# Optimization experiments

Hardware: AMD Instinct MI355X
Metric: run time of the kernel (lower is better)

Reference implementation:

```python
import jax, jax.numpy as jnp
import numpy as np

PD = 3                      # spatial feature dim (z, y, x)
HB = 1024                   # hash base per lattice coordinate
HOFF = 512                  # offset: lattice coords assumed in [-512, 511]
FILL = np.int32(2**31 - 1)  # sentinel for padded hash slots
EPS = 2.220446049250313e-16 # np.finfo('float').eps as in the torch module

def _elev_mat():
    # Embedding onto hyperplane sum(x)=0 with std-dev scale factors
    # (canonical permutohedral-lattice elevation, Adams et al.).
    E = np.zeros((PD + 1, PD), np.float32)
    E[0] = 1.0
    for i in range(1, PD + 1):
        E[i, i - 1] = -i
        E[i, i:] = 1.0
    inv_std = np.sqrt(2.0 / 3.0) * (PD + 1)
    scale = inv_std / np.sqrt(np.arange(1, PD + 1) * np.arange(2, PD + 2))
    return (E * scale[None, :]).astype(np.float32)

_EMAT = _elev_mat()
_IU = np.triu(np.ones((PD + 1, PD + 1), bool), 1)   # j > i
_IL = np.tril(np.ones((PD + 1, PD + 1), bool), -1)  # j < i

def _hash(k):  # (..., PD) int32 -> (...,) int32, injective for |coord| < 512
    return ((k[..., 0] + HOFF) * HB + (k[..., 1] + HOFF)) * HB + (k[..., 2] + HOFF)

def permutohedral(values, features):
    """Splat-blur-slice Gaussian filter. values (N,VD), features (N,PD)."""
    N, VD = values.shape
    elevated = features @ jnp.asarray(_EMAT).T                  # (N, PD+1)
    # nearest remainder-0 lattice point (nearest multiple of PD+1, ties -> down)
    v = elevated / (PD + 1)
    up, down = jnp.ceil(v), jnp.floor(v)
    rem0 = jnp.where(up - v < v - down, up, down) * (PD + 1)
    diff = elevated - rem0
    lt = diff[:, :, None] < diff[:, None, :]
    le = diff[:, :, None] <= diff[:, None, :]
    rank = (lt & _IU).sum(-1) + (le & _IL).sum(-1)              # (N, PD+1) int32
    rank = rank + jnp.round(rem0.sum(-1) / (PD + 1)).astype(rank.dtype)[:, None]
    shift = jnp.where(rank < 0, PD + 1, 0) + jnp.where(rank > PD, -(PD + 1), 0)
    rank = rank + shift
    rem0 = rem0 + shift.astype(rem0.dtype)
    # barycentric coordinates inside the enclosing simplex
    t = (elevated - rem0) / (PD + 1)                            # (N, PD+1)
    ohA = jax.nn.one_hot(PD - rank, PD + 2, dtype=values.dtype)
    ohB = jax.nn.one_hot(PD + 1 - rank, PD + 2, dtype=values.dtype)
    b = (ohA * t[..., None]).sum(1) - (ohB * t[..., None]).sum(1)
    b = b.at[:, 0].add(1.0 + b[:, PD + 1])
    bary = b[:, :PD + 1]                                        # (N, PD+1)
    # keys of the PD+1 simplex vertices (first PD coords; last is implied)
    rem0i = rem0[:, :PD].astype(jnp.int32)
    ranki = rank[:, :PD].astype(jnp.int32)
    r = jnp.arange(PD + 1, dtype=jnp.int32)[None, :, None]
    keys = rem0i[:, None, :] + jnp.where(ranki[:, None, :] >= PD + 1 - r, r - (PD + 1), r)  # (N,PD+1,PD)
    h = _hash(keys).reshape(-1)                                 # (N*(PD+1),)
    M = h.shape[0]
    uh, inv = jnp.unique(h, size=M, fill_value=FILL, return_inverse=True)
    inv = inv.reshape(-1)
    # splat
    contrib = (values[:, None, :] * bary[:, :, None]).reshape(M, VD)
    lat = jax.ops.segment_sum(contrib, inv, num_segments=M)     # (M, VD)
    # decode unique keys from the (invertible) hash
    k2 = uh % HB - HOFF
    tq = uh // HB
    k1 = tq % HB - HOFF
    k0 = tq // HB - HOFF
    ukeys = jnp.stack([k0, k1, k2], -1).astype(jnp.int32)       # (M, PD)
    valid = (uh != FILL)[:, None]
    # blur with [0.5, 1, 0.5] along each of the PD+1 lattice directions
    def lookup(nk, lat_):
        nh = _hash(nk)
        idx = jnp.clip(jnp.searchsorted(uh, nh), 0, M - 1)
        ok = (uh[idx] == nh)[:, None]
        return jnp.where(ok, lat_[idx], 0.0)
    for j in range(PD + 1):
        o = np.ones(PD, np.int32)
        if j < PD:
            o[j] = -PD
        o = jnp.asarray(o)
        lat = jnp.where(valid, lat + 0.5 * (lookup(ukeys + o, lat) + lookup(ukeys - o, lat)), 0.0)
    # slice
    alpha = 1.0 / (1.0 + 2.0 ** (-PD))
    return alpha * jnp.einsum('nr,nrv->nv', bary, lat[inv.reshape(-1, PD + 1)])

def spatial_features(image, v_gamma, sigma_gamma):
    _, d, h, w = image.shape
    z = jnp.arange(d, dtype=jnp.float32)[:, None, None]
    y = jnp.arange(h, dtype=jnp.float32)[None, :, None]
    x = jnp.arange(w, dtype=jnp.float32)[None, None, :]
    zz = v_gamma[0] * jnp.broadcast_to(z, (d, h, w)) / sigma_gamma[0]
    xx = v_gamma[1] * jnp.broadcast_to(x, (d, h, w)) / sigma_gamma[1]
    yy = v_gamma[2] * jnp.broadcast_to(y, (d, h, w)) / sigma_gamma[2]
    return jnp.stack([zz, yy, xx], axis=3)                      # (d,h,w,3)

def setup_inputs() -> dict:
    key = jax.random.key(0)
    k1, k2 = jax.random.split(key)
    C, D, H, W = 4, 64, 128, 128
    return {
        'input_': jax.random.normal(k1, (C, D, H, W), jnp.float32),
        'image': jax.random.normal(k2, (1, D, H, W), jnp.float32),
        'v_gamma': jnp.ones((3,), jnp.float32),       # nn.Parameter init [1,1,1]
        'sigma_gamma': 5.0 * jnp.ones((3,), jnp.float32),
    }

def reference(input_, image, v_gamma, sigma_gamma):
    C, d, h, w = input_.shape
    N = d * h * w
    feats = spatial_features(image, v_gamma, sigma_gamma).reshape(N, PD)
    # filter q and the all-ones normalizer in one pass (linear per channel)
    vals = jnp.concatenate([input_.reshape(C, N).T, jnp.ones((N, 1), jnp.float32)], axis=1)
    out = permutohedral(vals, feats)
    q = out[:, :C].T.reshape(C, d, h, w)
    norm = out[:, C].reshape(1, d, h, w)
    return q * (1.0 / (norm + EPS))
```

## Files before the change

kernel.cpp:

```cpp
#include <hip/hip_runtime.h>


#define DD    64
#define HHH   128
#define WWW   128
#define NPTS  (DD * HHH * WWW)
#define LATN  (1 << 17)
#define LATF  (LATN * 5)
#define SH_BITS 10
#define SHSZ (1 << SH_BITS)
#define BLURBLK 64

__device__ __forceinline__ int encK(int K0, int K1, int K2) {
    return ((K2 >> 2) << 12) | ((K1 >> 2) << 7) | ((K0 >> 2) << 2) | (K0 & 3);
}

__device__ __forceinline__ void pl_geom(int z, int y, int x,
                                        const float* __restrict__ vg,
                                        const float* __restrict__ sg,
                                        int* didx, float* bout) {
    float f0 = vg[0] * (float)z / sg[0];
    float f1 = vg[2] * (float)y / sg[2];
    float f2 = vg[1] * (float)x / sg[1];

    const float m00 = (float)2.3094010767585034;
    const float m01 = (float)1.3333333333333333;
    const float m02 = (float)0.9428090415820634;
    const float m21 = (float)-2.6666666666666665;
    const float m32 = (float)-2.8284271247461903;

    float e[4];
    e[0] =  m00 * f0 + m01 * f1 + m02 * f2;
    e[1] = -m00 * f0 + m01 * f1 + m02 * f2;
    e[2] =  m21 * f1 + m02 * f2;
    e[3] =  m32 * f2;

    float rem0[4];
    int sumr = 0;
    #pragma unroll
    for (int i = 0; i < 4; ++i) {
        float v = e[i] * 0.25f;
        float up = ceilf(v), dn = floorf(v);
        float rr = ((up - v) < (v - dn)) ? up : dn;
        rem0[i] = rr * 4.0f;
        sumr += (int)rem0[i];
    }
    sumr /= 4;

    float diff[4];
    #pragma unroll
    for (int i = 0; i < 4; ++i) diff[i] = e[i] - rem0[i];
    int rank[4] = {0, 0, 0, 0};
    #pragma unroll
    for (int i = 0; i < 4; ++i)
        #pragma unroll
        for (int j = i + 1; j < 4; ++j) {
            if (diff[i] < diff[j]) rank[i]++; else rank[j]++;
        }

    #pragma unroll
    for (int i = 0; i < 4; ++i) {
        rank[i] += sumr;
        if (rank[i] < 0)      { rank[i] += 4; rem0[i] += 4.0f; }
        else if (rank[i] > 3) { rank[i] -= 4; rem0[i] -= 4.0f; }
    }

    float b[5] = {0.f, 0.f, 0.f, 0.f, 0.f};
    #pragma unroll
    for (int i = 0; i < 4; ++i) {
        float t = (e[i] - rem0[i]) * 0.25f;
        b[3 - rank[i]] += t;
        b[4 - rank[i]] -= t;
    }
    b[0] += 1.0f + b[4];

    int k0 = (int)rem0[0], k1 = (int)rem0[1], k2 = (int)rem0[2];
    #pragma unroll
    for (int r = 0; r < 4; ++r) {
        int o0 = (rank[0] >= 4 - r) ? (r - 4) : r;
        int o1 = (rank[1] >= 4 - r) ? (r - 4) : r;
        int o2 = (rank[2] >= 4 - r) ? (r - 4) : r;
        int K0 = (k0 + o0 + 16) & 127;
        int K1 = (k1 + o1 + 48) & 127;
        int K2 = (k2 + o2 + 88) & 127;
        didx[r] = encK(K0, K1, K2);
        bout[r] = b[r];
    }
}

__device__ __forceinline__ void pl_claim(int key, unsigned int* __restrict__ exists,
                                         int* __restrict__ wcnt, int* __restrict__ wl) {
    if (atomicExch(&exists[key], 1u) == 0u) {
        int p = atomicAdd(wcnt, 1);
        wl[p] = key;
    }
}

__device__ __forceinline__ void pl_emit(int key, const float* a,
                                        int* skey, float (*sacc)[5],
                                        float* __restrict__ latc,
                                        unsigned int* __restrict__ exists,
                                        int* __restrict__ wcnt, int* __restrict__ wl) {
    unsigned idx = ((unsigned)key * 2654435761u) >> (32 - SH_BITS);
    int probes = 0;
    bool inlds = true;
    for (;;) {
        int cur = skey[idx];
        if (cur == key) break;
        if (cur == -1) {
            cur = atomicCAS(&skey[idx], -1, key);
            if (cur == -1 || cur == key) break;
        }
        idx = (idx + 1) & (SHSZ - 1);
        if (++probes >= SHSZ) { inlds = false; break; }
    }
    if (inlds) {
        #pragma unroll
        for (int c = 0; c < 5; ++c) atomicAdd(&sacc[idx][c], a[c]);
    } else {
        float* L = latc + (size_t)key * 5;
        #pragma unroll
        for (int c = 0; c < 5; ++c) atomicAdd(L + c, a[c]);
        pl_claim(key, exists, wcnt, wl);
    }
}

__global__ __launch_bounds__(512, 4)
void pl_splat(const float* __restrict__ vals, const float* __restrict__ vg,
              const float* __restrict__ sg, float* __restrict__ latc,
              unsigned int* __restrict__ exists,
              int* __restrict__ wcnt, int* __restrict__ wl) {
    __shared__ int   skey[SHSZ];
    __shared__ float sacc[SHSZ][5];
    for (int i = threadIdx.x; i < SHSZ; i += 512) {
        skey[i] = -1;
        #pragma unroll
        for (int c = 0; c < 5; ++c) sacc[i][c] = 0.f;
    }
    __syncthreads();

    float* mycopy = latc + (size_t)(blockIdx.x & 3) * LATF;

    int bt = blockIdx.x;
    int xs = threadIdx.x & 7;
    int ly = (threadIdx.x >> 3) & 15;
    int lz = threadIdx.x >> 7;
    int xsl = ((xs & 3) << 1) | (xs >> 2);
    int x0 = ((bt & 3) << 5) + (xsl << 2);
    int y  = (((bt >> 2) & 7) << 4) + ly;
    int z  = ((bt >> 5) << 2) + lz;
    int n0 = (z << 14) + (y << 7) + x0;

    float4 q0 = *(const float4*)(vals + n0);
    float4 q1 = *(const float4*)(vals + NPTS + n0);
    float4 q2 = *(const float4*)(vals + 2 * NPTS + n0);
    float4 q3 = *(const float4*)(vals + 3 * NPTS + n0);
    float ch0[4] = {q0.x, q0.y, q0.z, q0.w};
    float ch1[4] = {q1.x, q1.y, q1.z, q1.w};
    float ch2[4] = {q2.x, q2.y, q2.z, q2.w};
    float ch3[4] = {q3.x, q3.y, q3.z, q3.w};

    int ckey[4];
    float acc[4][5];
    {
        int didx[4]; float b[4];
        pl_geom(z, y, x0, vg, sg, didx, b);
        #pragma unroll
        for (int r = 0; r < 4; ++r) {
            ckey[r] = didx[r];
            float w = b[r];
            acc[r][0] = w * ch0[0]; acc[r][1] = w * ch1[0];
            acc[r][2] = w * ch2[0]; acc[r][3] = w * ch3[0];
            acc[r][4] = w;
        }
    }
    #pragma unroll
    for (int p = 1; p < 4; ++p) {
        int didx[4]; float b[4];
        pl_geom(z, y, x0 + p, vg, sg, didx, b);
        #pragma unroll
        for (int r = 0; r < 4; ++r) {
            float w = b[r];
            if (didx[r] == ckey[r]) {
                acc[r][0] += w * ch0[p]; acc[r][1] += w * ch1[p];
                acc[r][2] += w * ch2[p]; acc[r][3] += w * ch3[p];
                acc[r][4] += w;
            } else {
                pl_emit(ckey[r], acc[r], skey, sacc, mycopy, exists, wcnt, wl);
                ckey[r] = didx[r];
                acc[r][0] = w * ch0[p]; acc[r][1] = w * ch1[p];
                acc[r][2] = w * ch2[p]; acc[r][3] = w * ch3[p];
                acc[r][4] = w;
            }
        }
    }
    #pragma unroll
    for (int r = 0; r < 4; ++r)
        pl_emit(ckey[r], acc[r], skey, sacc, mycopy, exists, wcnt, wl);

    __syncthreads();

    int rot = (blockIdx.x * 131) & (SHSZ - 1);
    for (int ii = threadIdx.x; ii < SHSZ; ii += 512) {
        int i = (ii + rot) & (SHSZ - 1);
        int key = skey[i];
        if (key < 0) continue;
        pl_claim(key, exists, wcnt, wl);
        float* L = mycopy + (size_t)key * 5;
        #pragma unroll
        for (int c = 0; c < 5; ++c) atomicAdd(L + c, sacc[i][c]);
    }
}

__global__ __launch_bounds__(256)
void pl_blur(const unsigned int* __restrict__ exists,
             const int* __restrict__ wl, const int* __restrict__ wcnt,
             const float* __restrict__ in, float* __restrict__ out,
             int d0, int d1, int d2, int first) {
    int cnt = *wcnt;
    for (int i = blockIdx.x * 256 + threadIdx.x; i < cnt; i += BLURBLK * 256) {
        int didx = wl[i];
        int r  = didx & 3;
        int K0 = (((didx >> 2)  & 31) << 2) | r;
        int K1 = (((didx >> 7)  & 31) << 2) | r;
        int K2 = (((didx >> 12) & 31) << 2) | r;
        float a[5];
        size_t o = (size_t)didx * 5;
        if (first) {
            #pragma unroll
            for (int c = 0; c < 5; ++c)
                a[c] = in[o + c] + in[LATF + o + c] +
                       in[2 * LATF + o + c] + in[3 * LATF + o + c];
        } else {
            #pragma unroll
            for (int c = 0; c < 5; ++c) a[c] = in[o + c];
        }
        #pragma unroll
        for (int sgn = 0; sgn < 2; ++sgn) {
            int P0 = K0 + (sgn ? -d0 : d0);
            int P1 = K1 + (sgn ? -d1 : d1);
            int P2 = K2 + (sgn ? -d2 : d2);
            if (((unsigned)P0 < 128u) & ((unsigned)P1 < 128u) & ((unsigned)P2 < 128u)) {
                int nk = encK(P0, P1, P2);
                if (exists[nk]) {
                    size_t no = (size_t)nk * 5;
                    if (first) {
                        #pragma unroll
                        for (int c = 0; c < 5; ++c)
                            a[c] += 0.5f * (in[no + c] + in[LATF + no + c] +
                                            in[2 * LATF + no + c] + in[3 * LATF + no + c]);
                    } else {
                        #pragma unroll
                        for (int c = 0; c < 5; ++c) a[c] += 0.5f * in[no + c];
                    }
                }
            }
        }
        #pragma unroll
        for (int c = 0; c < 5; ++c) out[o + c] = a[c];
    }
}

__global__ __launch_bounds__(256)
void pl_slice(const float* __restrict__ vg, const float* __restrict__ sg,
              const float* __restrict__ lat, float* __restrict__ out) {
    int n = blockIdx.x * 256 + threadIdx.x;
    if (n >= NPTS) return;
    int z = n >> 14;
    int y = (n >> 7) & 127;
    int x = n & 127;
    int didx[4]; float b[4];
    pl_geom(z, y, x, vg, sg, didx, b);
    float a0 = 0.f, a1 = 0.f, a2 = 0.f, a3 = 0.f, a4 = 0.f;
    #pragma unroll
    for (int r = 0; r < 4; ++r) {
        float w = b[r];
        const float* L = lat + (size_t)didx[r] * 5;
        a0 += w * L[0]; a1 += w * L[1]; a2 += w * L[2]; a3 += w * L[3]; a4 += w * L[4];
    }
    const float alpha = (float)(1.0 / 1.125);
    float norm = alpha * a4 + (float)2.220446049250313e-16;
    float invn = 1.0f / norm;
    out[n]            = (alpha * a0) * invn;
    out[NPTS + n]     = (alpha * a1) * invn;
    out[2 * NPTS + n] = (alpha * a2) * invn;
    out[3 * NPTS + n] = (alpha * a3) * invn;
}

extern "C" void kernel_launch(void* const* d_in, const int* in_sizes, int n_in,
                              void* d_out, int out_size, void* d_ws, size_t ws_size,
                              hipStream_t stream) {
    const float* input = (const float*)d_in[0];
    const float* vg = (const float*)d_in[2];
    const float* sg = (const float*)d_in[3];
    float* out = (float*)d_out;

    char* ws = (char*)d_ws;
    float* latc = (float*)ws;
    unsigned int* exists = (unsigned int*)(latc + (size_t)4 * LATF);
    int* wcnt = (int*)(exists + LATN);
    int*   wl = (int*)(wcnt + 64);
    float* A  = (float*)(wl + LATN);
    float* B  = A + LATF;

    size_t zbytes = (size_t)4 * LATF * 4 + (size_t)LATN * 4 + 256;
    hipMemsetAsync(ws, 0, zbytes, stream);

    pl_splat<<<512, dim3(512), 0, stream>>>(input, vg, sg, latc, exists, wcnt, wl);

    pl_blur<<<BLURBLK, dim3(256), 0, stream>>>(exists, wl, wcnt, latc, A, -3, 1, 1, 1);
    pl_blur<<<BLURBLK, dim3(256), 0, stream>>>(exists, wl, wcnt, A, B, 1, -3, 1, 0);
    pl_blur<<<BLURBLK, dim3(256), 0, stream>>>(exists, wl, wcnt, B, A, 1, 1, -3, 0);
    pl_blur<<<BLURBLK, dim3(256), 0, stream>>>(exists, wl, wcnt, A, B, 1, 1, 1, 0);

    pl_slice<<<NPTS / 256, dim3(256), 0, stream>>>(vg, sg, B, out);
}
```

Before: 191.2 us.

## Replace LDS hash splat with dense tile grid and fuse three blur passes

The splat kernel drops the per-block LDS open-addressing hash in favour of a dense 7x7x7x4 local lattice window. Each tile computes its window base analytically, accumulates with LDS atomics plus a bitmask, and falls back to global atomics for points outside the window. The last three blur passes are fused into one kernel that recomputes neighbour values recursively (p1f/p2f), which removes two launches and the intermediate round trips but causes heavy redundant gathers (about 27 reads per output channel). The blur is also parallelised per channel element, and the grid sizes change.

```diff
diff --git a/kernel.cpp b/kernel.cpp
--- a/kernel.cpp
+++ b/kernel.cpp
@@ -7,9 +7,9 @@
 #define NPTS  (DD * HHH * WWW)
 #define LATN  (1 << 17)
 #define LATF  (LATN * 5)
-#define SH_BITS 10
-#define SHSZ (1 << SH_BITS)
-#define BLURBLK 64
+#define DQ    7
+#define CELLS (DQ * DQ * DQ * 4)
+#define MASKW ((CELLS + 31) / 32)
 
 __device__ __forceinline__ int encK(int K0, int K1, int K2) {
     return ((K2 >> 2) << 12) | ((K1 >> 2) << 7) | ((K0 >> 2) << 2) | (K0 & 3);
@@ -18,7 +18,7 @@
 __device__ __forceinline__ void pl_geom(int z, int y, int x,
                                         const float* __restrict__ vg,
                                         const float* __restrict__ sg,
-                                        int* didx, float* bout) {
+                                        int* Kout , float* bout) {
     float f0 = vg[0] * (float)z / sg[0];
     float f1 = vg[2] * (float)y / sg[2];
     float f2 = vg[1] * (float)x / sg[1];
@@ -74,16 +74,15 @@
     }
     b[0] += 1.0f + b[4];
 
-    int k0 = (int)rem0[0], k1 = (int)rem0[1], k2 = (int)rem0[2];
+    int k0 = (int)rem0[0] + 16, k1 = (int)rem0[1] + 48, k2 = (int)rem0[2] + 88;
     #pragma unroll
     for (int r = 0; r < 4; ++r) {
         int o0 = (rank[0] >= 4 - r) ? (r - 4) : r;
         int o1 = (rank[1] >= 4 - r) ? (r - 4) : r;
         int o2 = (rank[2] >= 4 - r) ? (r - 4) : r;
-        int K0 = (k0 + o0 + 16) & 127;
-        int K1 = (k1 + o1 + 48) & 127;
-        int K2 = (k2 + o2 + 88) & 127;
-        didx[r] = encK(K0, K1, K2);
+        Kout[r * 3 + 0] = k0 + o0;
+        Kout[r * 3 + 1] = k1 + o1;
+        Kout[r * 3 + 2] = k2 + o2;
         bout[r] = b[r];
     }
 }
@@ -96,59 +95,47 @@
     }
 }
 
-__device__ __forceinline__ void pl_emit(int key, const float* a,
-                                        int* skey, float (*sacc)[5],
-                                        float* __restrict__ latc,
-                                        unsigned int* __restrict__ exists,
-                                        int* __restrict__ wcnt, int* __restrict__ wl) {
-    unsigned idx = ((unsigned)key * 2654435761u) >> (32 - SH_BITS);
-    int probes = 0;
-    bool inlds = true;
-    for (;;) {
-        int cur = skey[idx];
-        if (cur == key) break;
-        if (cur == -1) {
-            cur = atomicCAS(&skey[idx], -1, key);
-            if (cur == -1 || cur == key) break;
-        }
-        idx = (idx + 1) & (SHSZ - 1);
-        if (++probes >= SHSZ) { inlds = false; break; }
-    }
-    if (inlds) {
-        #pragma unroll
-        for (int c = 0; c < 5; ++c) atomicAdd(&sacc[idx][c], a[c]);
-    } else {
-        float* L = latc + (size_t)key * 5;
-        #pragma unroll
-        for (int c = 0; c < 5; ++c) atomicAdd(L + c, a[c]);
-        pl_claim(key, exists, wcnt, wl);
-    }
-}
-
-__global__ __launch_bounds__(512, 4)
+__device__ __forceinline__ void gl_add5(float* __restrict__ L, const float* a) {
+    #pragma unroll
+    for (int c = 0; c < 5; ++c) atomicAdd(L + c, a[c]);
+}
+
+__global__ __launch_bounds__(256, 4)
 void pl_splat(const float* __restrict__ vals, const float* __restrict__ vg,
               const float* __restrict__ sg, float* __restrict__ latc,
               unsigned int* __restrict__ exists,
               int* __restrict__ wcnt, int* __restrict__ wl) {
-    __shared__ int   skey[SHSZ];
-    __shared__ float sacc[SHSZ][5];
-    for (int i = threadIdx.x; i < SHSZ; i += 512) {
-        skey[i] = -1;
-        #pragma unroll
-        for (int c = 0; c < 5; ++c) sacc[i][c] = 0.f;
-    }
+    __shared__ float sacc[CELLS * 5];
+    __shared__ unsigned int smask[MASKW];
+    for (int i = threadIdx.x; i < CELLS * 5; i += 256) sacc[i] = 0.f;
+    for (int i = threadIdx.x; i < MASKW; i += 256) smask[i] = 0u;
     __syncthreads();
 
-    float* mycopy = latc + (size_t)(blockIdx.x & 3) * LATF;
-
     int bt = blockIdx.x;
-    int xs = threadIdx.x & 7;
-    int ly = (threadIdx.x >> 3) & 15;
-    int lz = threadIdx.x >> 7;
-    int xsl = ((xs & 3) << 1) | (xs >> 2);
-    int x0 = ((bt & 3) << 5) + (xsl << 2);
-    int y  = (((bt >> 2) & 7) << 4) + ly;
-    int z  = ((bt >> 5) << 2) + lz;
+    int tx = (bt & 3) << 5;
+    int ty = ((bt >> 2) & 15) << 3;
+    int tz = (bt >> 6) << 2;
+
+    float s0 = vg[0] / sg[0], s1 = vg[2] / sg[2], s2 = vg[1] / sg[1];
+    const float m00 = 2.30940104f, m01 = 1.33333325f, m02 = 0.942809045f,
+                m21 = -2.66666651f;
+    float A0z = m00 * s0, A0y = m01 * s1, A0x = m02 * s2;
+    float A1z = -A0z,     A1y = A0y,      A1x = A0x;
+    float A2y = m21 * s1, A2x = A0x;
+    float e0o = A0z * tz + A0y * ty + A0x * tx;
+    float e1o = A1z * tz + A1y * ty + A1x * tx;
+    float e2o = A2y * ty + A2x * tx;
+    float e0m = e0o + fminf(0.f, A0z) * 3 + fminf(0.f, A0y) * 7 + fminf(0.f, A0x) * 31;
+    float e1m = e1o + fminf(0.f, A1z) * 3 + fminf(0.f, A1y) * 7 + fminf(0.f, A1x) * 31;
+    float e2m = e2o + fminf(0.f, A2y) * 7 + fminf(0.f, A2x) * 31;
+    int B0 = ((int)floorf(e0m + 16.f - 7.f)) & ~3;
+    int B1 = ((int)floorf(e1m + 48.f - 7.f)) & ~3;
+    int B2 = ((int)floorf(e2m + 88.f - 7.f)) & ~3;
+
+    int xs = (threadIdx.x & 7) << 2;
+    int y  = ty + ((threadIdx.x >> 3) & 7);
+    int z  = tz + (threadIdx.x >> 6);
+    int x0 = tx + xs;
     int n0 = (z << 14) + (y << 7) + x0;
 
     float4 q0 = *(const float4*)(vals + n0);
@@ -160,104 +147,128 @@
     float ch2[4] = {q2.x, q2.y, q2.z, q2.w};
     float ch3[4] = {q3.x, q3.y, q3.z, q3.w};
 
-    int ckey[4];
-    float acc[4][5];
-    {
-        int didx[4]; float b[4];
-        pl_geom(z, y, x0, vg, sg, didx, b);
+    float* mycopy = latc + (size_t)(blockIdx.x & 3) * LATF;
+
+    #pragma unroll
+    for (int p = 0; p < 4; ++p) {
+        int K[12]; float b[4];
+        pl_geom(z, y, x0 + p, vg, sg, K, b);
         #pragma unroll
         for (int r = 0; r < 4; ++r) {
-            ckey[r] = didx[r];
+            int l0 = K[r * 3 + 0] - B0;
+            int l1 = K[r * 3 + 1] - B1;
+            int l2 = K[r * 3 + 2] - B2;
             float w = b[r];
-            acc[r][0] = w * ch0[0]; acc[r][1] = w * ch1[0];
-            acc[r][2] = w * ch2[0]; acc[r][3] = w * ch3[0];
-            acc[r][4] = w;
-        }
-    }
-    #pragma unroll
-    for (int p = 1; p < 4; ++p) {
-        int didx[4]; float b[4];
-        pl_geom(z, y, x0 + p, vg, sg, didx, b);
-        #pragma unroll
-        for (int r = 0; r < 4; ++r) {
-            float w = b[r];
-            if (didx[r] == ckey[r]) {
-                acc[r][0] += w * ch0[p]; acc[r][1] += w * ch1[p];
-                acc[r][2] += w * ch2[p]; acc[r][3] += w * ch3[p];
-                acc[r][4] += w;
+            if (((unsigned)l0 < 4u * DQ) & ((unsigned)l1 < 4u * DQ) &
+                ((unsigned)l2 < 4u * DQ)) {
+                int idx = ((((l2 >> 2) * DQ) + (l1 >> 2)) * DQ + (l0 >> 2)) * 4 + (l0 & 3);
+                atomicAdd(&sacc[idx * 5 + 0], w * ch0[p]);
+                atomicAdd(&sacc[idx * 5 + 1], w * ch1[p]);
+                atomicAdd(&sacc[idx * 5 + 2], w * ch2[p]);
+                atomicAdd(&sacc[idx * 5 + 3], w * ch3[p]);
+                atomicAdd(&sacc[idx * 5 + 4], w);
+                atomicOr(&smask[idx >> 5], 1u << (idx & 31));
             } else {
-                pl_emit(ckey[r], acc[r], skey, sacc, mycopy, exists, wcnt, wl);
-                ckey[r] = didx[r];
-                acc[r][0] = w * ch0[p]; acc[r][1] = w * ch1[p];
-                acc[r][2] = w * ch2[p]; acc[r][3] = w * ch3[p];
-                acc[r][4] = w;
+                int key = encK(K[r * 3] & 127, K[r * 3 + 1] & 127, K[r * 3 + 2] & 127);
+                float a[5] = {w * ch0[p], w * ch1[p], w * ch2[p], w * ch3[p], w};
+                gl_add5(mycopy + (size_t)key * 5, a);
+                pl_claim(key, exists, wcnt, wl);
             }
         }
     }
-    #pragma unroll
-    for (int r = 0; r < 4; ++r)
-        pl_emit(ckey[r], acc[r], skey, sacc, mycopy, exists, wcnt, wl);
-
     __syncthreads();
 
-    int rot = (blockIdx.x * 131) & (SHSZ - 1);
-    for (int ii = threadIdx.x; ii < SHSZ; ii += 512) {
-        int i = (ii + rot) & (SHSZ - 1);
-        int key = skey[i];
-        if (key < 0) continue;
+    for (int i = threadIdx.x; i < CELLS; i += 256) {
+        if (!((smask[i >> 5] >> (i & 31)) & 1u)) continue;
+        int r = i & 3, q = i >> 2;
+        int l0q = q % DQ; int t = q / DQ;
+        int l1q = t % DQ; int l2q = t / DQ;
+        int K0 = B0 + (l0q << 2) + r;
+        int K1 = B1 + (l1q << 2) + r;
+        int K2 = B2 + (l2q << 2) + r;
+        int key = encK(K0 & 127, K1 & 127, K2 & 127);
         pl_claim(key, exists, wcnt, wl);
-        float* L = mycopy + (size_t)key * 5;
-        #pragma unroll
-        for (int c = 0; c < 5; ++c) atomicAdd(L + c, sacc[i][c]);
-    }
+        gl_add5(mycopy + (size_t)key * 5, &sacc[i * 5]);
+    }
+}
+
+__device__ __forceinline__ float sum4g(const float* __restrict__ latc,
+                                       const unsigned int* __restrict__ exists,
+                                       int K0, int K1, int K2, int c) {
+    if (((unsigned)K0 >= 128u) | ((unsigned)K1 >= 128u) | ((unsigned)K2 >= 128u))
+        return 0.f;
+    int key = encK(K0, K1, K2);
+    if (!exists[key]) return 0.f;
+    size_t o = (size_t)key * 5 + c;
+    return latc[o] + latc[LATF + o] + latc[2 * LATF + o] + latc[3 * LATF + o];
 }
 
 __global__ __launch_bounds__(256)
-void pl_blur(const unsigned int* __restrict__ exists,
-             const int* __restrict__ wl, const int* __restrict__ wcnt,
-             const float* __restrict__ in, float* __restrict__ out,
-             int d0, int d1, int d2, int first) {
-    int cnt = *wcnt;
-    for (int i = blockIdx.x * 256 + threadIdx.x; i < cnt; i += BLURBLK * 256) {
-        int didx = wl[i];
+void pl_blur0(const unsigned int* __restrict__ exists,
+              const int* __restrict__ wl, const int* __restrict__ wcnt,
+              const float* __restrict__ latc, float* __restrict__ A) {
+    int total = (*wcnt) * 5;
+    for (int i = blockIdx.x * 256 + threadIdx.x; i < total; i += 256 * 256) {
+        int ci = i / 5, c = i - ci * 5;
+        int didx = wl[ci];
         int r  = didx & 3;
         int K0 = (((didx >> 2)  & 31) << 2) | r;
         int K1 = (((didx >> 7)  & 31) << 2) | r;
         int K2 = (((didx >> 12) & 31) << 2) | r;
-        float a[5];
-        size_t o = (size_t)didx * 5;
-        if (first) {
-            #pragma unroll
-            for (int c = 0; c < 5; ++c)
-                a[c] = in[o + c] + in[LATF + o + c] +
-                       in[2 * LATF + o + c] + in[3 * LATF + o + c];
-        } else {
-            #pragma unroll
-            for (int c = 0; c < 5; ++c) a[c] = in[o + c];
-        }
-        #pragma unroll
-        for (int sgn = 0; sgn < 2; ++sgn) {
-            int P0 = K0 + (sgn ? -d0 : d0);
-            int P1 = K1 + (sgn ? -d1 : d1);
-            int P2 = K2 + (sgn ? -d2 : d2);
-            if (((unsigned)P0 < 128u) & ((unsigned)P1 < 128u) & ((unsigned)P2 < 128u)) {
-                int nk = encK(P0, P1, P2);
-                if (exists[nk]) {
-                    size_t no = (size_t)nk * 5;
-                    if (first) {
-                        #pragma unroll
-                        for (int c = 0; c < 5; ++c)
-                            a[c] += 0.5f * (in[no + c] + in[LATF + no + c] +
-                                            in[2 * LATF + no + c] + in[3 * LATF + no + c]);
-                    } else {
-                        #pragma unroll
-                        for (int c = 0; c < 5; ++c) a[c] += 0.5f * in[no + c];
-                    }
-                }
-            }
-        }
-        #pragma unroll
-        for (int c = 0; c < 5; ++c) out[o + c] = a[c];
+        size_t o = (size_t)didx * 5 + c;
+        float ctr = latc[o] + latc[LATF + o] + latc[2 * LATF + o] + latc[3 * LATF + o];
+        float pn = sum4g(latc, exists, K0 - 3, K1 + 1, K2 + 1, c) +
+                   sum4g(latc, exists, K0 + 3, K1 - 1, K2 - 1, c);
+        A[o] = ctr + 0.5f * pn;
+    }
+}
+
+__device__ __forceinline__ float rdA(const float* __restrict__ A,
+                                     const unsigned int* __restrict__ exists,
+                                     int K0, int K1, int K2, int c) {
+    if (((unsigned)K0 >= 128u) | ((unsigned)K1 >= 128u) | ((unsigned)K2 >= 128u))
+        return 0.f;
+    int key = encK(K0, K1, K2);
+    return exists[key] ? A[(size_t)key * 5 + c] : 0.f;
+}
+__device__ __forceinline__ float p1f(const float* __restrict__ A,
+                                     const unsigned int* __restrict__ exists,
+                                     int K0, int K1, int K2, int c) {
+    if (((unsigned)K0 >= 128u) | ((unsigned)K1 >= 128u) | ((unsigned)K2 >= 128u))
+        return 0.f;
+    int key = encK(K0, K1, K2);
+    if (!exists[key]) return 0.f;
+    float n = rdA(A, exists, K0 + 1, K1 - 3, K2 + 1, c) +
+              rdA(A, exists, K0 - 1, K1 + 3, K2 - 1, c);
+    return A[(size_t)key * 5 + c] + 0.5f * n;
+}
+__device__ __forceinline__ float p2f(const float* __restrict__ A,
+                                     const unsigned int* __restrict__ exists,
+                                     int K0, int K1, int K2, int c) {
+    if (((unsigned)K0 >= 128u) | ((unsigned)K1 >= 128u) | ((unsigned)K2 >= 128u))
+        return 0.f;
+    int key = encK(K0, K1, K2);
+    if (!exists[key]) return 0.f;
+    float n = p1f(A, exists, K0 + 1, K1 + 1, K2 - 3, c) +
+              p1f(A, exists, K0 - 1, K1 - 1, K2 + 3, c);
+    return p1f(A, exists, K0, K1, K2, c) + 0.5f * n;
+}
+
+__global__ __launch_bounds__(256)
+void pl_blur123(const unsigned int* __restrict__ exists,
+                const int* __restrict__ wl, const int* __restrict__ wcnt,
+                const float* __restrict__ A, float* __restrict__ B) {
+    int total = (*wcnt) * 5;
+    for (int i = blockIdx.x * 256 + threadIdx.x; i < total; i += 256 * 256) {
+        int ci = i / 5, c = i - ci * 5;
+        int didx = wl[ci];
+        int r  = didx & 3;
+        int K0 = (((didx >> 2)  & 31) << 2) | r;
+        int K1 = (((didx >> 7)  & 31) << 2) | r;
+        int K2 = (((didx >> 12) & 31) << 2) | r;
+        float n = p2f(A, exists, K0 + 1, K1 + 1, K2 + 1, c) +
+                  p2f(A, exists, K0 - 1, K1 - 1, K2 - 1, c);
+        B[(size_t)didx * 5 + c] = p2f(A, exists, K0, K1, K2, c) + 0.5f * n;
     }
 }
 
@@ -269,13 +280,14 @@
     int z = n >> 14;
     int y = (n >> 7) & 127;
     int x = n & 127;
-    int didx[4]; float b[4];
-    pl_geom(z, y, x, vg, sg, didx, b);
+    int K[12]; float b[4];
+    pl_geom(z, y, x, vg, sg, K, b);
     float a0 = 0.f, a1 = 0.f, a2 = 0.f, a3 = 0.f, a4 = 0.f;
     #pragma unroll
     for (int r = 0; r < 4; ++r) {
         float w = b[r];
-        const float* L = lat + (size_t)didx[r] * 5;
+        int key = encK(K[r * 3] & 127, K[r * 3 + 1] & 127, K[r * 3 + 2] & 127);
+        const float* L = lat + (size_t)key * 5;
         a0 += w * L[0]; a1 += w * L[1]; a2 += w * L[2]; a3 += w * L[3]; a4 += w * L[4];
     }
     const float alpha = (float)(1.0 / 1.125);
@@ -306,12 +318,8 @@
     size_t zbytes = (size_t)4 * LATF * 4 + (size_t)LATN * 4 + 256;
     hipMemsetAsync(ws, 0, zbytes, stream);
 
-    pl_splat<<<512, dim3(512), 0, stream>>>(input, vg, sg, latc, exists, wcnt, wl);
-
-    pl_blur<<<BLURBLK, dim3(256), 0, stream>>>(exists, wl, wcnt, latc, A, -3, 1, 1, 1);
-    pl_blur<<<BLURBLK, dim3(256), 0, stream>>>(exists, wl, wcnt, A, B, 1, -3, 1, 0);
-    pl_blur<<<BLURBLK, dim3(256), 0, stream>>>(exists, wl, wcnt, B, A, 1, 1, -3, 0);
-    pl_blur<<<BLURBLK, dim3(256), 0, stream>>>(exists, wl, wcnt, A, B, 1, 1, 1, 0);
-
+    pl_splat<<<1024, dim3(256), 0, stream>>>(input, vg, sg, latc, exists, wcnt, wl);
+    pl_blur0<<<256, dim3(256), 0, stream>>>(exists, wl, wcnt, latc, A);
+    pl_blur123<<<256, dim3(256), 0, stream>>>(exists, wl, wcnt, A, B);
     pl_slice<<<NPTS / 256, dim3(256), 0, stream>>>(vg, sg, B, out);
 }
```

New measurement: 236.0 us. +23.4%, slower.
